# Performance work log

Hardware: AMD Instinct MI355X
Metric: run time of the kernel (lower is better)

The kernel has to match this reference:

```python
import jax, jax.numpy as jnp
import numpy as np

B, T, D = 4, 2048, 1024
H = 16
DK = D // H

def setup_inputs() -> dict:
    key = jax.random.key(0)
    k1, k2, k3, k4, k5 = jax.random.split(key, 5)
    s = 1.0 / np.sqrt(D)
    return {
        "x": jax.random.normal(k1, (B, T, D), dtype=jnp.float32),
        # torch Linear convention: weight [out, in], y = x @ W.T + b
        "W_qkv": jax.random.uniform(k2, (3 * D, D), jnp.float32, -s, s),
        "b_qkv": jax.random.uniform(k3, (3 * D,), jnp.float32, -s, s),
        "W_proj": jax.random.uniform(k4, (D, D), jnp.float32, -s, s),
        "b_proj": jax.random.uniform(k5, (D,), jnp.float32, -s, s),
    }

def reference(x, W_qkv, b_qkv, W_proj, b_proj):
    Bx, Tx, C = x.shape
    qkv = x @ W_qkv.T + b_qkv                      # [B,T,3D]
    qkv = qkv.reshape(Bx, Tx, 3, H, DK)
    qkv = jnp.transpose(qkv, (2, 0, 3, 1, 4))      # [3,B,H,T,dk]
    q, k, v = qkv[0], qkv[1], qkv[2]
    att = jnp.einsum('bhqd,bhkd->bhqk', q, k) / np.sqrt(DK)
    causal = jnp.tril(jnp.ones((Tx, Tx), dtype=bool))
    att = jnp.where(causal[None, None], att, -jnp.inf)
    att = jax.nn.softmax(att, axis=-1)
    out = jnp.einsum('bhqk,bhkd->bhqd', att, v)    # [B,H,T,dk]
    out = jnp.transpose(out, (0, 2, 1, 3)).reshape(Bx, Tx, C)
    return out @ W_proj.T + b_proj
```

## Files before the change

### kernel.cpp

```cpp
#include <hip/hip_runtime.h>

typedef unsigned short ushort_t;
typedef __attribute__((ext_vector_type(8))) short short8;
typedef __attribute__((ext_vector_type(4))) float f32x4;

#define DEV __device__ __forceinline__

constexpr int B_ = 4, T_ = 2048, D_ = 1024, H_ = 16;
constexpr int M_ = B_ * T_;
constexpr float LOG2E_ = 1.4426950408889634f;

DEV ushort_t f2bf(float f) {
  union { float f; unsigned u; } c; c.f = f;
  unsigned u = c.u;
  return (ushort_t)((u + 0x7fffu + ((u >> 16) & 1u)) >> 16);
}
DEV float bf2f(ushort_t b) {
  union { unsigned u; float f; } c; c.u = ((unsigned)b) << 16;
  return c.f;
}
DEV unsigned cvt_pk_bf16(float lo, float hi) {
  unsigned r;
  asm("v_cvt_pk_bf16_f32 %0, %1, %2" : "=v"(r) : "v"(lo), "v"(hi));
  return r;
}

DEV void gload_lds16(const void* g, void* l) {
  __builtin_amdgcn_global_load_lds(
      (const __attribute__((address_space(1))) void*)g,
      (__attribute__((address_space(3))) void*)l, 16, 0, 0);
}

__global__ void __launch_bounds__(256) f2bf_kernel(
    const float* __restrict__ in, ushort_t* __restrict__ out, int n4) {
  int stride = gridDim.x * blockDim.x;
  for (int i = blockIdx.x * blockDim.x + threadIdx.x; i < n4; i += stride) {
    float4 v = reinterpret_cast<const float4*>(in)[i];
    ushort4 o;
    o.x = f2bf(v.x); o.y = f2bf(v.y); o.z = f2bf(v.z); o.w = f2bf(v.w);
    reinterpret_cast<ushort4*>(out)[i] = o;
  }
}

template <bool OUT_BF16>
__global__ void __launch_bounds__(256) gemm_bt(
    const ushort_t* __restrict__ A, const ushort_t* __restrict__ Bw,
    const float* __restrict__ bias, void* __restrict__ Cout,
    ushort_t* __restrict__ VT, int M, int N, int K, int ldc) {
  __shared__ __align__(16) ushort_t lA[128 * 64];
  __shared__ __align__(16) ushort_t lB[128 * 64];
  const int tid = threadIdx.x;
  const int lane = tid & 63;
  const int w = tid >> 6;
  const int wm = w >> 1, wn = w & 1;
  const int r0 = lane & 15;
  const int g8 = (lane >> 4) * 8;

  const int gx = gridDim.x;
  const int lin = blockIdx.y * gx + blockIdx.x;
  const int cpx = (gx * gridDim.y) >> 3;
  const int swz = (lin & 7) * cpx + (lin >> 3);
  const int m0 = (swz / gx) * 128, n0 = (swz % gx) * 128;

  f32x4 acc[4][4] = {};

  for (int k0 = 0; k0 < K; k0 += 64) {
    int flat = tid * 8;
    for (int it = 0; it < 4; ++it) {
      int f = it * 2048 + flat;
      int row = f >> 6, col = f & 63;
      gload_lds16(A + (size_t)(m0 + row) * K + k0 + col, &lA[f]);
      gload_lds16(Bw + (size_t)(n0 + row) * K + k0 + col, &lB[f]);
    }
    __syncthreads();
    __builtin_amdgcn_s_setprio(1);
    for (int kc = 0; kc < 64; kc += 32) {
      short8 aF[4], bF[4];
      for (int mi = 0; mi < 4; ++mi)
        aF[mi] = *(const short8*)&lA[(wm * 64 + mi * 16 + r0) * 64 + kc + g8];
      for (int ni = 0; ni < 4; ++ni)
        bF[ni] = *(const short8*)&lB[(wn * 64 + ni * 16 + r0) * 64 + kc + g8];
      for (int mi = 0; mi < 4; ++mi)
        for (int ni = 0; ni < 4; ++ni)
          acc[mi][ni] = __builtin_amdgcn_mfma_f32_16x16x32_bf16(
              aF[mi], bF[ni], acc[mi][ni], 0, 0, 0);
    }
    __builtin_amdgcn_s_setprio(0);
    __syncthreads();
  }

  const int rg = (lane >> 4) * 4;
  const bool vpath = (VT != nullptr) && (n0 >= 2048);
  if (vpath) {
    for (int mi = 0; mi < 4; ++mi)
      for (int ni = 0; ni < 4; ++ni) {
        int n = n0 + wn * 64 + ni * 16 + r0;
        float bv = bias[n];
        int vcol = n - 2048;
        int hh = vcol >> 6, dd = vcol & 63;
        int m = m0 + wm * 64 + mi * 16 + rg;
        int bb = m >> 11, tt = m & 2047;
        ushort4 o;
        o.x = f2bf(acc[mi][ni][0] + bv);
        o.y = f2bf(acc[mi][ni][1] + bv);
        o.z = f2bf(acc[mi][ni][2] + bv);
        o.w = f2bf(acc[mi][ni][3] + bv);
        *reinterpret_cast<ushort4*>(
            &VT[((size_t)((bb << 4) + hh) * 64 + dd) * (size_t)T_ + tt]) = o;
      }
  } else {
    for (int mi = 0; mi < 4; ++mi)
      for (int ni = 0; ni < 4; ++ni) {
        int n = n0 + wn * 64 + ni * 16 + r0;
        float bv = bias[n];
        for (int r = 0; r < 4; ++r) {
          int m = m0 + wm * 64 + mi * 16 + rg + r;
          float v = acc[mi][ni][r] + bv;
          if (OUT_BF16)
            ((ushort_t*)Cout)[(size_t)m * ldc + n] = f2bf(v);
          else
            ((float*)Cout)[(size_t)m * ldc + n] = v;
        }
      }
  }
}

__global__ void __launch_bounds__(256) attn_kernel(
    const ushort_t* __restrict__ qk, const ushort_t* __restrict__ Vt,
    ushort_t* __restrict__ O) {
  __shared__ __align__(16) ushort_t lK[2][64 * 64];
  __shared__ __align__(16) ushort_t lVT[2][64 * 64];
  __shared__ __align__(16) ushort_t lP[4][16 * 64];

  const int tid = threadIdx.x;
  const int lane = tid & 63;
  const int w = tid >> 6;
  const int r0 = lane & 15;
  const int p = lane >> 4;
  const int g8 = p * 8;
  const int rg = p * 4;

  const int lin = (int)blockIdx.y * 16 + (int)blockIdx.x;
  const int xcd = lin & 7;
  const int chunk = lin >> 3;
  const int bh = xcd * 8 + (chunk >> 4);
  const int pair = chunk & 15;

  const int b = bh >> 4, h = bh & 15;
  const float QSC = 0.125f * LOG2E_;

  const short8 bOne = {0x3F80, 0x3F80, 0x3F80, 0x3F80,
                       0x3F80, 0x3F80, 0x3F80, 0x3F80};

  ushort_t* lPw = &lP[w][0];

  const int f0 = tid * 8;
  const int row0 = f0 >> 6;
  const int lch0 = ((f0 >> 3) & 7) ^ (row0 & 7);
  const int f1 = 2048 + tid * 8;
  const int row1 = f1 >> 6;
  const int lch1 = ((f1 >> 3) & 7) ^ (row1 & 7);

  for (int half = 0; half < 2; ++half) {
    const int qblk = half ? (31 - pair) : pair;
    const int q0w = qblk * 64 + w * 16;

    short8 aQ[2];
#pragma unroll
    for (int kc = 0; kc < 2; ++kc) {
      short8 raw = *(const short8*)(qk + (size_t)(b * T_ + q0w + r0) * 2048 +
                                    h * 64 + kc * 32 + g8);
      short8 sc;
#pragma unroll
      for (int j = 0; j < 4; ++j) {
        float e0 = bf2f((ushort_t)raw[2 * j]) * QSC;
        float e1 = bf2f((ushort_t)raw[2 * j + 1]) * QSC;
        unsigned pk = cvt_pk_bf16(e0, e1);
        sc[2 * j] = (short)(ushort_t)pk;
        sc[2 * j + 1] = (short)(ushort_t)(pk >> 16);
      }
      aQ[kc] = sc;
    }

    f32x4 accO[4] = {};
    f32x4 accL = {};

    __syncthreads();
    {
      const ushort_t* kb = qk + (size_t)(b * T_) * 2048 + 1024 + h * 64;
      const ushort_t* vb = Vt + (size_t)bh * 64 * (size_t)T_;
      gload_lds16(kb + (size_t)row0 * 2048 + lch0 * 8, &lK[0][f0]);
      gload_lds16(kb + (size_t)row1 * 2048 + lch1 * 8, &lK[0][f1]);
      gload_lds16(vb + (size_t)row0 * T_ + lch0 * 8, &lVT[0][f0]);
      gload_lds16(vb + (size_t)row1 * T_ + lch1 * 8, &lVT[0][f1]);
    }
    int cur = 0;

    for (int kt = 0; kt <= qblk; ++kt) {
      __syncthreads();

      if (kt < qblk) {
        const ushort_t* kb =
            qk + (size_t)(b * T_ + (kt + 1) * 64) * 2048 + 1024 + h * 64;
        const ushort_t* vb =
            Vt + (size_t)bh * 64 * (size_t)T_ + (kt + 1) * 64;
        ushort_t* dK = &lK[cur ^ 1][0];
        ushort_t* dV = &lVT[cur ^ 1][0];
        gload_lds16(kb + (size_t)row0 * 2048 + lch0 * 8, dK + f0);
        gload_lds16(kb + (size_t)row1 * 2048 + lch1 * 8, dK + f1);
        gload_lds16(vb + (size_t)row0 * T_ + lch0 * 8, dV + f0);
        gload_lds16(vb + (size_t)row1 * T_ + lch1 * 8, dV + f1);
      }

      const ushort_t* bufK = &lK[cur][0];
      const ushort_t* bufV = &lVT[cur][0];

      f32x4 sA[4];
#pragma unroll
      for (int ni = 0; ni < 4; ++ni)
        sA[ni] = f32x4{-16.f, -16.f, -16.f, -16.f};
      __builtin_amdgcn_s_setprio(1);
#pragma unroll
      for (int kc = 0; kc < 2; ++kc)
#pragma unroll
        for (int ni = 0; ni < 4; ++ni) {
          int row = ni * 16 + r0;
          int ch = (kc * 4 + p) ^ (row & 7);
          short8 bK = *(const short8*)&bufK[row * 64 + ch * 8];
          sA[ni] = __builtin_amdgcn_mfma_f32_16x16x32_bf16(aQ[kc], bK, sA[ni], 0, 0, 0);
        }
      __builtin_amdgcn_s_setprio(0);

      if (kt == qblk) {
#pragma unroll
        for (int ni = 0; ni < 4; ++ni) {
          if (ni > w) {
#pragma unroll
            for (int r = 0; r < 4; ++r) sA[ni][r] = -1e30f;
          } else if (ni == w) {
#pragma unroll
            for (int r = 0; r < 4; ++r)
              if (r0 > rg + r) sA[ni][r] = -1e30f;
          }
        }
      }

#pragma unroll
      for (int ni = 0; ni < 4; ++ni) {
        float p0 = exp2f(sA[ni][0]);
        float p1 = exp2f(sA[ni][1]);
        float p2 = exp2f(sA[ni][2]);
        float p3 = exp2f(sA[ni][3]);
        unsigned lo = cvt_pk_bf16(p0, p1);
        unsigned hi = cvt_pk_bf16(p2, p3);
        int col = ni * 16 + r0;
#pragma unroll
        for (int r = 0; r < 4; ++r) {
          int rowp = rg + r;
          ushort_t hw = (r == 0)   ? (ushort_t)lo
                        : (r == 1) ? (ushort_t)(lo >> 16)
                        : (r == 2) ? (ushort_t)hi
                                   : (ushort_t)(hi >> 16);
          lPw[rowp * 64 + (col ^ ((rowp & 7) << 3))] = hw;
        }
      }

      __builtin_amdgcn_s_setprio(1);
#pragma unroll
      for (int kc = 0; kc < 2; ++kc) {
        int pch = (kc * 4 + p) ^ (r0 & 7);
        short8 aP = *(const short8*)&lPw[r0 * 64 + pch * 8];
        accL = __builtin_amdgcn_mfma_f32_16x16x32_bf16(aP, bOne, accL, 0, 0, 0);
#pragma unroll
        for (int ni = 0; ni < 4; ++ni) {
          int row = ni * 16 + r0;
          int ch = (kc * 4 + p) ^ (row & 7);
          short8 bV = *(const short8*)&bufV[row * 64 + ch * 8];
          accO[ni] = __builtin_amdgcn_mfma_f32_16x16x32_bf16(aP, bV, accO[ni], 0, 0, 0);
        }
      }
      __builtin_amdgcn_s_setprio(0);
      cur ^= 1;
    }

#pragma unroll
    for (int ni = 0; ni < 4; ++ni)
#pragma unroll
      for (int r = 0; r < 4; ++r) {
        int q = q0w + rg + r;
        float v = accO[ni][r] / accL[r];
        O[(size_t)(b * T_ + q) * 1024 + h * 64 + ni * 16 + r0] = f2bf(v);
      }
  }
}

extern "C" void kernel_launch(void* const* d_in, const int* in_sizes, int n_in,
                              void* d_out, int out_size, void* d_ws, size_t ws_size,
                              hipStream_t stream) {
  const float* x = (const float*)d_in[0];
  const float* Wqkv = (const float*)d_in[1];
  const float* bqkv = (const float*)d_in[2];
  const float* Wproj = (const float*)d_in[3];
  const float* bproj = (const float*)d_in[4];
  float* out = (float*)d_out;

  ushort_t* xb = (ushort_t*)d_ws;
  ushort_t* wqkvb = xb + (size_t)M_ * D_;
  ushort_t* wprojb = wqkvb + (size_t)3 * D_ * D_;
  ushort_t* qkb = wprojb + (size_t)D_ * D_;
  ushort_t* Vt = qkb + (size_t)M_ * 2048;
  ushort_t* Ob = Vt + (size_t)M_ * D_;

  f2bf_kernel<<<2048, 256, 0, stream>>>(x, xb, M_ * D_ / 4);
  f2bf_kernel<<<2048, 256, 0, stream>>>(Wqkv, wqkvb, 3 * D_ * D_ / 4);
  f2bf_kernel<<<1024, 256, 0, stream>>>(Wproj, wprojb, D_ * D_ / 4);

  gemm_bt<true><<<dim3(24, 64), 256, 0, stream>>>(
      xb, wqkvb, bqkv, qkb, Vt, M_, 3 * D_, D_, 2048);

  attn_kernel<<<dim3(16, 64), 256, 0, stream>>>(qkb, Vt, Ob);

  gemm_bt<false><<<dim3(8, 64), 256, 0, stream>>>(
      Ob, wprojb, bproj, out, nullptr, M_, D_, D_, D_);
}
```

Measured before the change: 214.3 us.

## Process both causal query blocks in one KV sweep and merge conversion kernels

The attention kernel now handles its two paired query blocks (pair and 31-pair) at the same time. It streams K/V tiles once over the longer range and reuses each loaded tile for both blocks, where before the short block's tiles were loaded twice. The three fp32-to-bf16 conversion launches are merged into one kernel, and attn_kernel gets a launch_bounds occupancy hint of 4. In exchange, registers per thread rise because there are two sets of Q fragments and accumulators, which could spill or cut occupancy.

```diff
diff --git a/kernel.cpp b/kernel.cpp
--- a/kernel.cpp
+++ b/kernel.cpp
@@ -31,14 +31,27 @@
       (__attribute__((address_space(3))) void*)l, 16, 0, 0);
 }
 
-__global__ void __launch_bounds__(256) f2bf_kernel(
-    const float* __restrict__ in, ushort_t* __restrict__ out, int n4) {
+__global__ void __launch_bounds__(256) f2bf3_kernel(
+    const float* __restrict__ a, ushort_t* __restrict__ oa, int na4,
+    const float* __restrict__ b, ushort_t* __restrict__ ob, int nb4,
+    const float* __restrict__ c, ushort_t* __restrict__ oc, int nc4) {
   int stride = gridDim.x * blockDim.x;
-  for (int i = blockIdx.x * blockDim.x + threadIdx.x; i < n4; i += stride) {
-    float4 v = reinterpret_cast<const float4*>(in)[i];
+  int ntot = na4 + nb4 + nc4;
+  for (int i = blockIdx.x * blockDim.x + threadIdx.x; i < ntot; i += stride) {
+    const float* src;
+    ushort_t* dst;
+    int j = i;
+    if (j < na4) {
+      src = a; dst = oa;
+    } else if (j < na4 + nb4) {
+      j -= na4; src = b; dst = ob;
+    } else {
+      j -= na4 + nb4; src = c; dst = oc;
+    }
+    float4 v = reinterpret_cast<const float4*>(src)[j];
     ushort4 o;
     o.x = f2bf(v.x); o.y = f2bf(v.y); o.z = f2bf(v.z); o.w = f2bf(v.w);
-    reinterpret_cast<ushort4*>(out)[i] = o;
+    reinterpret_cast<ushort4*>(dst)[j] = o;
   }
 }
 
@@ -125,7 +138,7 @@
   }
 }
 
-__global__ void __launch_bounds__(256) attn_kernel(
+__global__ void __launch_bounds__(256, 4) attn_kernel(
     const ushort_t* __restrict__ qk, const ushort_t* __restrict__ Vt,
     ushort_t* __restrict__ O) {
   __shared__ __align__(16) ushort_t lK[2][64 * 64];
@@ -161,64 +174,141 @@
   const int row1 = f1 >> 6;
   const int lch1 = ((f1 >> 3) & 7) ^ (row1 & 7);
 
-  for (int half = 0; half < 2; ++half) {
-    const int qblk = half ? (31 - pair) : pair;
-    const int q0w = qblk * 64 + w * 16;
-
-    short8 aQ[2];
+  const int qb1 = pair;
+  const int qb2 = 31 - pair;
+  const int q1 = qb1 * 64 + w * 16;
+  const int q2 = qb2 * 64 + w * 16;
+
+  short8 aQ1[2], aQ2[2];
+#pragma unroll
+  for (int kc = 0; kc < 2; ++kc) {
+    short8 raw1 = *(const short8*)(qk + (size_t)(b * T_ + q1 + r0) * 2048 +
+                                   h * 64 + kc * 32 + g8);
+    short8 raw2 = *(const short8*)(qk + (size_t)(b * T_ + q2 + r0) * 2048 +
+                                   h * 64 + kc * 32 + g8);
+    short8 s1, s2;
+#pragma unroll
+    for (int j = 0; j < 4; ++j) {
+      unsigned pk1 = cvt_pk_bf16(bf2f((ushort_t)raw1[2 * j]) * QSC,
+                                 bf2f((ushort_t)raw1[2 * j + 1]) * QSC);
+      unsigned pk2 = cvt_pk_bf16(bf2f((ushort_t)raw2[2 * j]) * QSC,
+                                 bf2f((ushort_t)raw2[2 * j + 1]) * QSC);
+      s1[2 * j] = (short)(ushort_t)pk1;
+      s1[2 * j + 1] = (short)(ushort_t)(pk1 >> 16);
+      s2[2 * j] = (short)(ushort_t)pk2;
+      s2[2 * j + 1] = (short)(ushort_t)(pk2 >> 16);
+    }
+    aQ1[kc] = s1;
+    aQ2[kc] = s2;
+  }
+
+  f32x4 accO1[4] = {}, accO2[4] = {};
+  f32x4 accL1 = {}, accL2 = {};
+
+  {
+    const ushort_t* kb = qk + (size_t)(b * T_) * 2048 + 1024 + h * 64;
+    const ushort_t* vb = Vt + (size_t)bh * 64 * (size_t)T_;
+    gload_lds16(kb + (size_t)row0 * 2048 + lch0 * 8, &lK[0][f0]);
+    gload_lds16(kb + (size_t)row1 * 2048 + lch1 * 8, &lK[0][f1]);
+    gload_lds16(vb + (size_t)row0 * T_ + lch0 * 8, &lVT[0][f0]);
+    gload_lds16(vb + (size_t)row1 * T_ + lch1 * 8, &lVT[0][f1]);
+  }
+  int cur = 0;
+
+  auto procPV = [&](f32x4* sA, const ushort_t* bufV, f32x4* accO,
+                    f32x4& accL) {
+#pragma unroll
+    for (int ni = 0; ni < 4; ++ni) {
+      float p0 = exp2f(sA[ni][0]);
+      float p1 = exp2f(sA[ni][1]);
+      float p2 = exp2f(sA[ni][2]);
+      float p3 = exp2f(sA[ni][3]);
+      unsigned lo = cvt_pk_bf16(p0, p1);
+      unsigned hi = cvt_pk_bf16(p2, p3);
+      int col = ni * 16 + r0;
+#pragma unroll
+      for (int r = 0; r < 4; ++r) {
+        int rowp = rg + r;
+        ushort_t hw = (r == 0)   ? (ushort_t)lo
+                      : (r == 1) ? (ushort_t)(lo >> 16)
+                      : (r == 2) ? (ushort_t)hi
+                                 : (ushort_t)(hi >> 16);
+        lPw[rowp * 64 + (col ^ ((rowp & 7) << 3))] = hw;
+      }
+    }
+    __builtin_amdgcn_s_setprio(1);
 #pragma unroll
     for (int kc = 0; kc < 2; ++kc) {
-      short8 raw = *(const short8*)(qk + (size_t)(b * T_ + q0w + r0) * 2048 +
-                                    h * 64 + kc * 32 + g8);
-      short8 sc;
-#pragma unroll
-      for (int j = 0; j < 4; ++j) {
-        float e0 = bf2f((ushort_t)raw[2 * j]) * QSC;
-        float e1 = bf2f((ushort_t)raw[2 * j + 1]) * QSC;
-        unsigned pk = cvt_pk_bf16(e0, e1);
-        sc[2 * j] = (short)(ushort_t)pk;
-        sc[2 * j + 1] = (short)(ushort_t)(pk >> 16);
-      }
-      aQ[kc] = sc;
-    }
-
-    f32x4 accO[4] = {};
-    f32x4 accL = {};
-
+      int pch = (kc * 4 + p) ^ (r0 & 7);
+      short8 aP = *(const short8*)&lPw[r0 * 64 + pch * 8];
+      accL = __builtin_amdgcn_mfma_f32_16x16x32_bf16(aP, bOne, accL, 0, 0, 0);
+#pragma unroll
+      for (int ni = 0; ni < 4; ++ni) {
+        int row = ni * 16 + r0;
+        int ch = (kc * 4 + p) ^ (row & 7);
+        short8 bV = *(const short8*)&bufV[row * 64 + ch * 8];
+        accO[ni] =
+            __builtin_amdgcn_mfma_f32_16x16x32_bf16(aP, bV, accO[ni], 0, 0, 0);
+      }
+    }
+    __builtin_amdgcn_s_setprio(0);
+  };
+
+  for (int kt = 0; kt <= qb2; ++kt) {
     __syncthreads();
-    {
-      const ushort_t* kb = qk + (size_t)(b * T_) * 2048 + 1024 + h * 64;
-      const ushort_t* vb = Vt + (size_t)bh * 64 * (size_t)T_;
-      gload_lds16(kb + (size_t)row0 * 2048 + lch0 * 8, &lK[0][f0]);
-      gload_lds16(kb + (size_t)row1 * 2048 + lch1 * 8, &lK[0][f1]);
-      gload_lds16(vb + (size_t)row0 * T_ + lch0 * 8, &lVT[0][f0]);
-      gload_lds16(vb + (size_t)row1 * T_ + lch1 * 8, &lVT[0][f1]);
-    }
-    int cur = 0;
-
-    for (int kt = 0; kt <= qblk; ++kt) {
-      __syncthreads();
-
-      if (kt < qblk) {
-        const ushort_t* kb =
-            qk + (size_t)(b * T_ + (kt + 1) * 64) * 2048 + 1024 + h * 64;
-        const ushort_t* vb =
-            Vt + (size_t)bh * 64 * (size_t)T_ + (kt + 1) * 64;
-        ushort_t* dK = &lK[cur ^ 1][0];
-        ushort_t* dV = &lVT[cur ^ 1][0];
-        gload_lds16(kb + (size_t)row0 * 2048 + lch0 * 8, dK + f0);
-        gload_lds16(kb + (size_t)row1 * 2048 + lch1 * 8, dK + f1);
-        gload_lds16(vb + (size_t)row0 * T_ + lch0 * 8, dV + f0);
-        gload_lds16(vb + (size_t)row1 * T_ + lch1 * 8, dV + f1);
-      }
-
-      const ushort_t* bufK = &lK[cur][0];
-      const ushort_t* bufV = &lVT[cur][0];
-
-      f32x4 sA[4];
+
+    if (kt < qb2) {
+      const ushort_t* kb =
+          qk + (size_t)(b * T_ + (kt + 1) * 64) * 2048 + 1024 + h * 64;
+      const ushort_t* vb = Vt + (size_t)bh * 64 * (size_t)T_ + (kt + 1) * 64;
+      ushort_t* dK = &lK[cur ^ 1][0];
+      ushort_t* dV = &lVT[cur ^ 1][0];
+      gload_lds16(kb + (size_t)row0 * 2048 + lch0 * 8, dK + f0);
+      gload_lds16(kb + (size_t)row1 * 2048 + lch1 * 8, dK + f1);
+      gload_lds16(vb + (size_t)row0 * T_ + lch0 * 8, dV + f0);
+      gload_lds16(vb + (size_t)row1 * T_ + lch1 * 8, dV + f1);
+    }
+
+    const ushort_t* bufK = &lK[cur][0];
+    const ushort_t* bufV = &lVT[cur][0];
+    const bool act1 = (kt <= qb1);
+
+    f32x4 sA2[4];
+#pragma unroll
+    for (int ni = 0; ni < 4; ++ni)
+      sA2[ni] = f32x4{-16.f, -16.f, -16.f, -16.f};
+    __builtin_amdgcn_s_setprio(1);
+#pragma unroll
+    for (int kc = 0; kc < 2; ++kc)
+#pragma unroll
+      for (int ni = 0; ni < 4; ++ni) {
+        int row = ni * 16 + r0;
+        int ch = (kc * 4 + p) ^ (row & 7);
+        short8 bK = *(const short8*)&bufK[row * 64 + ch * 8];
+        sA2[ni] =
+            __builtin_amdgcn_mfma_f32_16x16x32_bf16(aQ2[kc], bK, sA2[ni], 0, 0, 0);
+      }
+    __builtin_amdgcn_s_setprio(0);
+    if (kt == qb2) {
+#pragma unroll
+      for (int ni = 0; ni < 4; ++ni) {
+        if (ni > w) {
+#pragma unroll
+          for (int r = 0; r < 4; ++r) sA2[ni][r] = -1e30f;
+        } else if (ni == w) {
+#pragma unroll
+          for (int r = 0; r < 4; ++r)
+            if (r0 > rg + r) sA2[ni][r] = -1e30f;
+        }
+      }
+    }
+    procPV(sA2, bufV, accO2, accL2);
+
+    if (act1) {
+      f32x4 sA1[4];
 #pragma unroll
       for (int ni = 0; ni < 4; ++ni)
-        sA[ni] = f32x4{-16.f, -16.f, -16.f, -16.f};
+        sA1[ni] = f32x4{-16.f, -16.f, -16.f, -16.f};
       __builtin_amdgcn_s_setprio(1);
 #pragma unroll
       for (int kc = 0; kc < 2; ++kc)
@@ -227,71 +317,39 @@
           int row = ni * 16 + r0;
           int ch = (kc * 4 + p) ^ (row & 7);
           short8 bK = *(const short8*)&bufK[row * 64 + ch * 8];
-          sA[ni] = __builtin_amdgcn_mfma_f32_16x16x32_bf16(aQ[kc], bK, sA[ni], 0, 0, 0);
+          sA1[ni] = __builtin_amdgcn_mfma_f32_16x16x32_bf16(aQ1[kc], bK,
+                                                            sA1[ni], 0, 0, 0);
         }
       __builtin_amdgcn_s_setprio(0);
-
-      if (kt == qblk) {
+      if (kt == qb1) {
 #pragma unroll
         for (int ni = 0; ni < 4; ++ni) {
           if (ni > w) {
 #pragma unroll
-            for (int r = 0; r < 4; ++r) sA[ni][r] = -1e30f;
+            for (int r = 0; r < 4; ++r) sA1[ni][r] = -1e30f;
           } else if (ni == w) {
 #pragma unroll
             for (int r = 0; r < 4; ++r)
-              if (r0 > rg + r) sA[ni][r] = -1e30f;
+              if (r0 > rg + r) sA1[ni][r] = -1e30f;
           }
         }
       }
-
-#pragma unroll
-      for (int ni = 0; ni < 4; ++ni) {
-        float p0 = exp2f(sA[ni][0]);
-        float p1 = exp2f(sA[ni][1]);
-        float p2 = exp2f(sA[ni][2]);
-        float p3 = exp2f(sA[ni][3]);
-        unsigned lo = cvt_pk_bf16(p0, p1);
-        unsigned hi = cvt_pk_bf16(p2, p3);
-        int col = ni * 16 + r0;
-#pragma unroll
-        for (int r = 0; r < 4; ++r) {
-          int rowp = rg + r;
-          ushort_t hw = (r == 0)   ? (ushort_t)lo
-                        : (r == 1) ? (ushort_t)(lo >> 16)
-                        : (r == 2) ? (ushort_t)hi
-                                   : (ushort_t)(hi >> 16);
-          lPw[rowp * 64 + (col ^ ((rowp & 7) << 3))] = hw;
-        }
-      }
-
-      __builtin_amdgcn_s_setprio(1);
-#pragma unroll
-      for (int kc = 0; kc < 2; ++kc) {
-        int pch = (kc * 4 + p) ^ (r0 & 7);
-        short8 aP = *(const short8*)&lPw[r0 * 64 + pch * 8];
-        accL = __builtin_amdgcn_mfma_f32_16x16x32_bf16(aP, bOne, accL, 0, 0, 0);
-#pragma unroll
-        for (int ni = 0; ni < 4; ++ni) {
-          int row = ni * 16 + r0;
-          int ch = (kc * 4 + p) ^ (row & 7);
-          short8 bV = *(const short8*)&bufV[row * 64 + ch * 8];
-          accO[ni] = __builtin_amdgcn_mfma_f32_16x16x32_bf16(aP, bV, accO[ni], 0, 0, 0);
-        }
-      }
-      __builtin_amdgcn_s_setprio(0);
-      cur ^= 1;
-    }
-
-#pragma unroll
-    for (int ni = 0; ni < 4; ++ni)
-#pragma unroll
-      for (int r = 0; r < 4; ++r) {
-        int q = q0w + rg + r;
-        float v = accO[ni][r] / accL[r];
-        O[(size_t)(b * T_ + q) * 1024 + h * 64 + ni * 16 + r0] = f2bf(v);
-      }
-  }
+      procPV(sA1, bufV, accO1, accL1);
+    }
+
+    cur ^= 1;
+  }
+
+#pragma unroll
+  for (int ni = 0; ni < 4; ++ni)
+#pragma unroll
+    for (int r = 0; r < 4; ++r) {
+      int d = h * 64 + ni * 16 + r0;
+      float v1 = accO1[ni][r] / accL1[r];
+      float v2 = accO2[ni][r] / accL2[r];
+      O[(size_t)(b * T_ + q1 + rg + r) * 1024 + d] = f2bf(v1);
+      O[(size_t)(b * T_ + q2 + rg + r) * 1024 + d] = f2bf(v2);
+    }
 }
 
 extern "C" void kernel_launch(void* const* d_in, const int* in_sizes, int n_in,
@@ -311,9 +369,10 @@
   ushort_t* Vt = qkb + (size_t)M_ * 2048;
   ushort_t* Ob = Vt + (size_t)M_ * D_;
 
-  f2bf_kernel<<<2048, 256, 0, stream>>>(x, xb, M_ * D_ / 4);
-  f2bf_kernel<<<2048, 256, 0, stream>>>(Wqkv, wqkvb, 3 * D_ * D_ / 4);
-  f2bf_kernel<<<1024, 256, 0, stream>>>(Wproj, wprojb, D_ * D_ / 4);
+  f2bf3_kernel<<<2048, 256, 0, stream>>>(
+      x, xb, M_ * D_ / 4,
+      Wqkv, wqkvb, 3 * D_ * D_ / 4,
+      Wproj, wprojb, D_ * D_ / 4);
 
   gemm_bt<true><<<dim3(24, 64), 256, 0, stream>>>(
       xb, wqkvb, bqkv, qkb, Vt, M_, 3 * D_, D_, 2048);
```

Measured after the change: 195.4 us. 8.8% less time.
